# Optimization experiments

Measured on AMD Instinct MI355X. Metric: run time of the kernel, lower is better.

Reference implementation:

```python
import jax, jax.numpy as jnp
import numpy as np


def setup_inputs() -> dict:
    key = jax.random.key(0)
    k1, k2, k3 = jax.random.split(key, 3)
    H, W, C = 200, 200, 512
    NUM_ROIS = 300
    img = jax.random.normal(k1, (1, H, W, C), dtype=jnp.float32)
    # rois[0, r] = (x, y, w, h); ensure crops are in-bounds and non-empty
    xy = jax.random.randint(k2, (1, NUM_ROIS, 2), 0, 100)
    wh = jax.random.randint(k3, (1, NUM_ROIS, 2), 1, 100)
    rois = jnp.concatenate([xy, wh], axis=-1).astype(jnp.int32)
    return {"img": img, "rois": rois, "pool_size": 7}


def reference(img, rois, pool_size):
    """RoiPoolingConv: per-ROI crop + legacy-TF bilinear resize, vectorized.

    img:  [1, H, W, C] float feature map
    rois: [1, R, 4] int (x, y, w, h) in feature-map pixels
    returns [1, R, P, P, C]
    """
    P = pool_size
    img0 = img[0]                              # [H, W, C]
    H, W, C = img0.shape
    x = rois[0, :, 0].astype(jnp.int32)        # [R]
    y = rois[0, :, 1].astype(jnp.int32)
    w = rois[0, :, 2].astype(jnp.int32)
    h = rois[0, :, 3].astype(jnp.int32)

    out_idx = jnp.arange(P, dtype=jnp.float32)  # [P]
    # legacy tf.image.resize_images (bilinear, align_corners=False):
    #   src = out_idx * (in_size / out_size); corners floor(src), floor(src)+1 clipped
    sy = y[:, None].astype(jnp.float32) + out_idx[None, :] * (h[:, None].astype(jnp.float32) / P)  # [R,P]
    sx = x[:, None].astype(jnp.float32) + out_idx[None, :] * (w[:, None].astype(jnp.float32) / P)  # [R,P]

    y0 = jnp.floor(sy).astype(jnp.int32)
    x0 = jnp.floor(sx).astype(jnp.int32)
    y1 = jnp.minimum(y0 + 1, y[:, None] + h[:, None] - 1)  # clip to crop bottom edge
    x1 = jnp.minimum(x0 + 1, x[:, None] + w[:, None] - 1)
    # safety clamp to image bounds
    y0 = jnp.clip(y0, 0, H - 1); y1 = jnp.clip(y1, 0, H - 1)
    x0 = jnp.clip(x0, 0, W - 1); x1 = jnp.clip(x1, 0, W - 1)

    wy = (sy - jnp.floor(sy))[:, :, None, None]  # [R,P,1,1]
    wx = (sx - jnp.floor(sx))[:, None, :, None]  # [R,1,P,1]

    # gather the 4 corners for all ROIs at once -> [R,P,P,C]
    v00 = img0[y0[:, :, None], x0[:, None, :]]
    v01 = img0[y0[:, :, None], x1[:, None, :]]
    v10 = img0[y1[:, :, None], x0[:, None, :]]
    v11 = img0[y1[:, :, None], x1[:, None, :]]

    top = v00 * (1.0 - wx) + v01 * wx
    bot = v10 * (1.0 - wx) + v11 * wx
    out = top * (1.0 - wy) + bot * wy          # [R,P,P,C]
    return out[None]                           # [1,R,P,P,C]
```

## Files before the change

kernel.cpp:

```cpp
#include <hip/hip_runtime.h>
#include <hip/hip_bf16.h>
#include <cmath>


__global__ __launch_bounds__(256) void roi_pool_kernel(
    const float* __restrict__ img, const int* __restrict__ rois,
    float* __restrict__ out, int P, int H, int W, int C) {
  const int b = blockIdx.x;
  const int pp = P * P;
  const int r = b / pp;
  const int ij = b - r * pp;
  const int i = ij / P;
  const int j = ij - i * P;

  const int x = rois[r * 4 + 0];
  const int y = rois[r * 4 + 1];
  const int w = rois[r * 4 + 2];
  const int h = rois[r * 4 + 3];

  const float Pf = (float)P;
  const float sy = (float)y + (float)i * ((float)h / Pf);
  const float sx = (float)x + (float)j * ((float)w / Pf);
  const float fy = floorf(sy);
  const float fx = floorf(sx);
  int y0 = (int)fy;
  int x0 = (int)fx;
  int y1 = min(y0 + 1, y + h - 1);
  int x1 = min(x0 + 1, x + w - 1);
  y0 = min(max(y0, 0), H - 1);
  y1 = min(max(y1, 0), H - 1);
  x0 = min(max(x0, 0), W - 1);
  x1 = min(max(x1, 0), W - 1);
  const float wy = sy - fy;
  const float wx = sx - fx;
  const float omwx = 1.0f - wx;
  const float omwy = 1.0f - wy;

  const float* __restrict__ p00 = img + ((size_t)y0 * W + x0) * C;
  const float* __restrict__ p01 = img + ((size_t)y0 * W + x1) * C;
  const float* __restrict__ p10 = img + ((size_t)y1 * W + x0) * C;
  const float* __restrict__ p11 = img + ((size_t)y1 * W + x1) * C;
  float* __restrict__ po = out + (size_t)b * C;

  for (int c = threadIdx.x * 2; c < C; c += blockDim.x * 2) {
    const float2 v00 = *reinterpret_cast<const float2*>(p00 + c);
    const float2 v01 = *reinterpret_cast<const float2*>(p01 + c);
    const float2 v10 = *reinterpret_cast<const float2*>(p10 + c);
    const float2 v11 = *reinterpret_cast<const float2*>(p11 + c);
    float2 o;
    {
      const float top = v00.x * omwx + v01.x * wx;
      const float bot = v10.x * omwx + v11.x * wx;
      o.x = top * omwy + bot * wy;
    }
    {
      const float top = v00.y * omwx + v01.y * wx;
      const float bot = v10.y * omwx + v11.y * wx;
      o.y = top * omwy + bot * wy;
    }
    *reinterpret_cast<float2*>(po + c) = o;
  }
}

extern "C" void kernel_launch(void* const* d_in, const int* in_sizes, int n_in,
                              void* d_out, int out_size, void* d_ws, size_t ws_size,
                              hipStream_t stream) {
  const float* img = (const float*)d_in[0];
  const int* rois = (const int*)d_in[1];
  float* out = (float*)d_out;

  const int H = 200, W = 200, C = 512;
  const int R = in_sizes[1] / 4;
  const int pp = out_size / (R * C);
  int P = 1;
  while ((P + 1) * (P + 1) <= pp) ++P;

  const int blocks = R * pp;
  roi_pool_kernel<<<blocks, 256, 0, stream>>>(img, rois, out, P, H, W, C);
}
```

Measured before the change: 25.03 us.

## Map one block per ROI row with one wavefront per output column

Each block now handles a whole output row (i) of one ROI, and each 64-lane wavefront handles one output column j. This cuts the grid from R*P*P blocks to R*P blocks. Each lane processes 8 channels with two float4 loads per corner instead of float2 loads, so one pass covers all 512 channels. The block size becomes P*64 with launch bounds raised to 448, which assumes P<=7. Larger P would exceed the bound.

```diff
diff --git a/kernel.cpp b/kernel.cpp
--- a/kernel.cpp
+++ b/kernel.cpp
@@ -3,15 +3,14 @@
 #include <cmath>
 
 
-__global__ __launch_bounds__(256) void roi_pool_kernel(
+__global__ __launch_bounds__(448) void roi_pool_kernel(
     const float* __restrict__ img, const int* __restrict__ rois,
     float* __restrict__ out, int P, int H, int W, int C) {
   const int b = blockIdx.x;
-  const int pp = P * P;
-  const int r = b / pp;
-  const int ij = b - r * pp;
-  const int i = ij / P;
-  const int j = ij - i * P;
+  const int r = b / P;
+  const int i = b - r * P;
+  const int j = threadIdx.x >> 6;
+  const int lane = threadIdx.x & 63;
 
   const int x = rois[r * 4 + 0];
   const int y = rois[r * 4 + 1];
@@ -40,25 +39,43 @@
   const float* __restrict__ p01 = img + ((size_t)y0 * W + x1) * C;
   const float* __restrict__ p10 = img + ((size_t)y1 * W + x0) * C;
   const float* __restrict__ p11 = img + ((size_t)y1 * W + x1) * C;
-  float* __restrict__ po = out + (size_t)b * C;
+  float* __restrict__ po = out + ((size_t)b * P + j) * C;
 
-  for (int c = threadIdx.x * 2; c < C; c += blockDim.x * 2) {
-    const float2 v00 = *reinterpret_cast<const float2*>(p00 + c);
-    const float2 v01 = *reinterpret_cast<const float2*>(p01 + c);
-    const float2 v10 = *reinterpret_cast<const float2*>(p10 + c);
-    const float2 v11 = *reinterpret_cast<const float2*>(p11 + c);
-    float2 o;
-    {
-      const float top = v00.x * omwx + v01.x * wx;
-      const float bot = v10.x * omwx + v11.x * wx;
-      o.x = top * omwy + bot * wy;
+  for (int c = lane * 8; c < C; c += 64 * 8) {
+    const float4 a00 = *reinterpret_cast<const float4*>(p00 + c);
+    const float4 b00 = *reinterpret_cast<const float4*>(p00 + c + 4);
+    const float4 a01 = *reinterpret_cast<const float4*>(p01 + c);
+    const float4 b01 = *reinterpret_cast<const float4*>(p01 + c + 4);
+    const float4 a10 = *reinterpret_cast<const float4*>(p10 + c);
+    const float4 b10 = *reinterpret_cast<const float4*>(p10 + c + 4);
+    const float4 a11 = *reinterpret_cast<const float4*>(p11 + c);
+    const float4 b11 = *reinterpret_cast<const float4*>(p11 + c + 4);
+
+    float4 oa, ob;
+#define LERP1(F, v00_, v01_, v10_, v11_)                      \
+    {                                                          \
+      const float top = v00_.F * omwx + v01_.F * wx;           \
+      const float bot = v10_.F * omwx + v11_.F * wx;           \
+      oa.F = top * omwy + bot * wy;                            \
     }
-    {
-      const float top = v00.y * omwx + v01.y * wx;
-      const float bot = v10.y * omwx + v11.y * wx;
-      o.y = top * omwy + bot * wy;
+#define LERP2(F, v00_, v01_, v10_, v11_)                      \
+    {                                                          \
+      const float top = v00_.F * omwx + v01_.F * wx;           \
+      const float bot = v10_.F * omwx + v11_.F * wx;           \
+      ob.F = top * omwy + bot * wy;                            \
     }
-    *reinterpret_cast<float2*>(po + c) = o;
+    LERP1(x, a00, a01, a10, a11)
+    LERP1(y, a00, a01, a10, a11)
+    LERP1(z, a00, a01, a10, a11)
+    LERP1(w, a00, a01, a10, a11)
+    LERP2(x, b00, b01, b10, b11)
+    LERP2(y, b00, b01, b10, b11)
+    LERP2(z, b00, b01, b10, b11)
+    LERP2(w, b00, b01, b10, b11)
+#undef LERP1
+#undef LERP2
+    *reinterpret_cast<float4*>(po + c) = oa;
+    *reinterpret_cast<float4*>(po + c + 4) = ob;
   }
 }
 
@@ -75,6 +92,6 @@
   int P = 1;
   while ((P + 1) * (P + 1) <= pp) ++P;
 
-  const int blocks = R * pp;
-  roi_pool_kernel<<<blocks, 256, 0, stream>>>(img, rois, out, P, H, W, C);
+  const int blocks = R * P;
+  roi_pool_kernel<<<blocks, P * 64, 0, stream>>>(img, rois, out, P, H, W, C);
 }
```

New measurement: 24.89 us. No clear change (-0.5%).

## Map one wavefront per output pixel and skip redundant corner loads

Applied to the files above, without the earlier changes.

Reassigns work so each 64-lane wavefront handles one output pixel with two float4 loads per lane, packing four pixels per block. It also skips loading neighbor corners when the interpolation weight is zero or when clamped corners coincide, reusing already-loaded values. This aims to reduce read traffic and per-thread overhead, at the cost of more branching and slightly different NaN/inf propagation when a weight is exactly zero.

```diff
diff --git a/kernel.cpp b/kernel.cpp
--- a/kernel.cpp
+++ b/kernel.cpp
@@ -5,28 +5,28 @@
 
 __global__ __launch_bounds__(256) void roi_pool_kernel(
     const float* __restrict__ img, const int* __restrict__ rois,
-    float* __restrict__ out, int P, int H, int W, int C) {
-  const int b = blockIdx.x;
+    float* __restrict__ out, int P, int H, int W, int C, int npix) {
+  const int g = blockIdx.x * 4 + (threadIdx.x >> 6);
+  if (g >= npix) return;
+  const int lane = threadIdx.x & 63;
   const int pp = P * P;
-  const int r = b / pp;
-  const int ij = b - r * pp;
+  const int r = g / pp;
+  const int ij = g - r * pp;
   const int i = ij / P;
   const int j = ij - i * P;
 
-  const int x = rois[r * 4 + 0];
-  const int y = rois[r * 4 + 1];
-  const int w = rois[r * 4 + 2];
-  const int h = rois[r * 4 + 3];
+  const int4 roi = *reinterpret_cast<const int4*>(rois + r * 4);
+  const int x = roi.x, y = roi.y, wd = roi.z, ht = roi.w;
 
   const float Pf = (float)P;
-  const float sy = (float)y + (float)i * ((float)h / Pf);
-  const float sx = (float)x + (float)j * ((float)w / Pf);
+  const float sy = (float)y + (float)i * ((float)ht / Pf);
+  const float sx = (float)x + (float)j * ((float)wd / Pf);
   const float fy = floorf(sy);
   const float fx = floorf(sx);
   int y0 = (int)fy;
   int x0 = (int)fx;
-  int y1 = min(y0 + 1, y + h - 1);
-  int x1 = min(x0 + 1, x + w - 1);
+  int y1 = min(y0 + 1, y + ht - 1);
+  int x1 = min(x0 + 1, x + wd - 1);
   y0 = min(max(y0, 0), H - 1);
   y1 = min(max(y1, 0), H - 1);
   x0 = min(max(x0, 0), W - 1);
@@ -35,31 +35,77 @@
   const float wx = sx - fx;
   const float omwx = 1.0f - wx;
   const float omwy = 1.0f - wy;
+  const bool xnz = (wx != 0.0f);
+  const bool ynz = (wy != 0.0f);
 
   const float* __restrict__ p00 = img + ((size_t)y0 * W + x0) * C;
   const float* __restrict__ p01 = img + ((size_t)y0 * W + x1) * C;
   const float* __restrict__ p10 = img + ((size_t)y1 * W + x0) * C;
   const float* __restrict__ p11 = img + ((size_t)y1 * W + x1) * C;
-  float* __restrict__ po = out + (size_t)b * C;
+  float* __restrict__ po = out + (size_t)g * C;
 
-  for (int c = threadIdx.x * 2; c < C; c += blockDim.x * 2) {
-    const float2 v00 = *reinterpret_cast<const float2*>(p00 + c);
-    const float2 v01 = *reinterpret_cast<const float2*>(p01 + c);
-    const float2 v10 = *reinterpret_cast<const float2*>(p10 + c);
-    const float2 v11 = *reinterpret_cast<const float2*>(p11 + c);
-    float2 o;
-    {
-      const float top = v00.x * omwx + v01.x * wx;
-      const float bot = v10.x * omwx + v11.x * wx;
-      o.x = top * omwy + bot * wy;
+#define LERP4(dst, lo, hi, wlo, whi)          \
+  dst.x = lo.x * wlo + hi.x * whi;            \
+  dst.y = lo.y * wlo + hi.y * whi;            \
+  dst.z = lo.z * wlo + hi.z * whi;            \
+  dst.w = lo.w * wlo + hi.w * whi;
+
+  for (int c = lane * 8; c < C; c += 64 * 8) {
+    const float4 a00 = *reinterpret_cast<const float4*>(p00 + c);
+    const float4 b00 = *reinterpret_cast<const float4*>(p00 + c + 4);
+
+    float4 a01, b01;
+    float4 ta, tb;
+    if (xnz) {
+      if (x1 != x0) {
+        a01 = *reinterpret_cast<const float4*>(p01 + c);
+        b01 = *reinterpret_cast<const float4*>(p01 + c + 4);
+      } else {
+        a01 = a00; b01 = b00;
+      }
+      LERP4(ta, a00, a01, omwx, wx)
+      LERP4(tb, b00, b01, omwx, wx)
+    } else {
+      ta = a00; tb = b00;
     }
-    {
-      const float top = v00.y * omwx + v01.y * wx;
-      const float bot = v10.y * omwx + v11.y * wx;
-      o.y = top * omwy + bot * wy;
+
+    float4 oa, ob;
+    if (ynz) {
+      float4 a10, b10;
+      if (y1 != y0) {
+        a10 = *reinterpret_cast<const float4*>(p10 + c);
+        b10 = *reinterpret_cast<const float4*>(p10 + c + 4);
+      } else {
+        a10 = a00; b10 = b00;
+      }
+      float4 ba, bb;
+      if (xnz) {
+        float4 a11, b11;
+        if (x1 != x0) {
+          if (y1 != y0) {
+            a11 = *reinterpret_cast<const float4*>(p11 + c);
+            b11 = *reinterpret_cast<const float4*>(p11 + c + 4);
+          } else {
+            a11 = a01; b11 = b01;
+          }
+        } else {
+          a11 = a10; b11 = b10;
+        }
+        LERP4(ba, a10, a11, omwx, wx)
+        LERP4(bb, b10, b11, omwx, wx)
+      } else {
+        ba = a10; bb = b10;
+      }
+      LERP4(oa, ta, ba, omwy, wy)
+      LERP4(ob, tb, bb, omwy, wy)
+    } else {
+      oa = ta; ob = tb;
     }
-    *reinterpret_cast<float2*>(po + c) = o;
+
+    *reinterpret_cast<float4*>(po + c) = oa;
+    *reinterpret_cast<float4*>(po + c + 4) = ob;
   }
+#undef LERP4
 }
 
 extern "C" void kernel_launch(void* const* d_in, const int* in_sizes, int n_in,
@@ -75,6 +121,7 @@
   int P = 1;
   while ((P + 1) * (P + 1) <= pp) ++P;
 
-  const int blocks = R * pp;
-  roi_pool_kernel<<<blocks, 256, 0, stream>>>(img, rois, out, P, H, W, C);
+  const int npix = R * pp;
+  const int blocks = (npix + 3) / 4;
+  roi_pool_kernel<<<blocks, 256, 0, stream>>>(img, rois, out, P, H, W, C, npix);
 }
```

Measured after the change: 22.16 us. 1.13x faster.
